# Kernel optimization log

Hardware: AMD Instinct MI355X
Metric: run time of the kernel (lower is better)

The kernel has to match this reference:

```python
import jax, jax.numpy as jnp
import numpy as np

DIM_X = 128
DIM_H = 128
HIDDEN = 512
BATCH = 4096


def _vf(x, h, t, W1, b1, W2, b2):
    # cfg vector field: 2-layer tanh MLP on concat([x, h, t]) -> (B, dim_x)
    B = x.shape[0]
    tcol = jnp.broadcast_to(jnp.reshape(t, (1, 1)), (B, 1)).astype(x.dtype)
    z = jnp.concatenate([x, h, tcol], axis=-1)  # (B, dim_x+dim_h+1)
    return jnp.tanh(z @ W1 + b1) @ W2 + b2  # (B, dim_x)


def _divergence(x, h, t, W1, b1, W2, b2):
    # Exact Jacobian trace: sum_i d v_i / d x_i, via dim_x forward-mode JVP
    # passes (replaces the torch per-dim reverse-mode autograd.grad loop).
    f = lambda xx: _vf(xx, h, t, W1, b1, W2, b2)
    dim = x.shape[1]

    def diag_i(i):
        e = jnp.zeros((dim,), x.dtype).at[i].set(1.0)
        _, tang = jax.jvp(f, (x,), (jnp.broadcast_to(e, x.shape),))  # (B, dim)
        return jnp.take(tang, i, axis=1)  # (B,)

    diag = jax.vmap(diag_i)(jnp.arange(dim))  # (dim, B)
    return jnp.sum(diag, axis=0)[:, None]  # (B, 1)


def setup_inputs() -> dict:
    key = jax.random.key(0)
    ks = jax.random.split(key, 9)
    return {
        "state": jax.random.normal(ks[0], (BATCH, DIM_X + 1), jnp.float32),
        "h": jax.random.normal(ks[1], (BATCH, DIM_H), jnp.float32),
        "h_null": jax.random.normal(ks[2], (BATCH, DIM_H), jnp.float32),
        "t": jax.random.uniform(ks[3], (1,), jnp.float32),
        "guidance_scale": jax.random.uniform(ks[4], (1,), jnp.float32),
        "W1": jax.random.normal(ks[5], (DIM_X + DIM_H + 1, HIDDEN), jnp.float32) * 0.05,
        "b1": jax.random.normal(ks[6], (HIDDEN,), jnp.float32) * 0.05,
        "W2": jax.random.normal(ks[7], (HIDDEN, DIM_X), jnp.float32) * 0.05,
        "b2": jax.random.normal(ks[8], (DIM_X,), jnp.float32) * 0.05,
    }


def reference(state, h, h_null, t, guidance_scale, W1, b1, W2, b2):
    x_t = state[:, :-1]  # (B, dim_x)
    gs = guidance_scale[0]
    v_h = _vf(x_t, h, t, W1, b1, W2, b2)
    v_h_null = _vf(x_t, h_null, t, W1, b1, W2, b2)
    v = (1.0 - gs) * v_h_null + gs * v_h
    div_h = _divergence(x_t, h, t, W1, b1, W2, b2)
    div_h_null = _divergence(x_t, h_null, t, W1, b1, W2, b2)
    div = (1.0 - gs) * div_h_null + gs * div_h
    return jnp.concatenate([v, div], axis=1)  # (B, dim_x+1)
```

## Files before the change

### kernel.cpp

```cpp
#include <hip/hip_runtime.h>
#include <hip/hip_bf16.h>

#define DX 128
#define DH 128
#define HID 512
#define NB 4096
#define ROWS 16
#define OUTC 129

typedef __attribute__((ext_vector_type(4))) float f32x4;
typedef __attribute__((ext_vector_type(4))) float float4v;
typedef __attribute__((ext_vector_type(2))) float float2v;
typedef __attribute__((ext_vector_type(8))) short bf16x8;
typedef __attribute__((ext_vector_type(4))) short bf16x4;
typedef __attribute__((ext_vector_type(2))) short bf16x2;

__device__ inline short f2bf(float f) {
    unsigned u = __float_as_uint(f);
    unsigned r = (u + 0x7fffu + ((u >> 16) & 1u)) >> 16;
    return (short)r;
}

__device__ inline float fast_tanh(float x) {
    float e = __expf(2.0f * x);
    float r = __builtin_amdgcn_rcpf(e + 1.0f);
    return 1.0f - 2.0f * r;
}

__global__ __launch_bounds__(256) void prep_kernel(
    const float* __restrict__ W1, const float* __restrict__ W2,
    float* __restrict__ c, short* __restrict__ w1p, short* __restrict__ w2p)
{
    __shared__ float tile[4][32][17];

    const int tid  = threadIdx.x;
    const int lane = tid & 63;
    const int w    = tid >> 6;
    const int l15  = lane & 15;
    const int l4   = lane >> 4;
    const int W    = blockIdx.x * 4 + w;

    if (W < 256) {
        int nt = W >> 3, ks = W & 7;
        int m0 = ks * 32, n0 = nt * 16;
        #pragma unroll
        for (int p = 0; p < 8; ++p) {
            int r = p * 4 + l4;
            tile[w][r][l15] = W1[(m0 + r) * HID + n0 + l15];
        }
    } else if (W < 384) {
        int idx = W - 256;
        int nt = idx >> 4, ks = idx & 15;
        int k0 = ks * 32, n0 = nt * 16;
        #pragma unroll
        for (int p = 0; p < 8; ++p) {
            int r = p * 4 + l4;
            tile[w][r][l15] = W2[(k0 + r) * DX + n0 + l15];
        }
    }
    __syncthreads();

    if (W < 256) {
        bf16x8 v;
        #pragma unroll
        for (int e = 0; e < 8; ++e) v[e] = f2bf(tile[w][l4 * 8 + e][l15]);
        *(bf16x8*)&w1p[W * 512 + lane * 8] = v;
    } else if (W < 384) {
        int idx = W - 256;
        bf16x8 v;
        #pragma unroll
        for (int e = 0; e < 8; ++e) v[e] = f2bf(tile[w][l4 * 8 + e][l15]);
        *(bf16x8*)&w2p[idx * 512 + lane * 8] = v;
    } else if (W < 896) {
        int k = W - 384;
        float p = W1[lane * HID + k] * W2[k * DX + lane]
                + W1[(lane + 64) * HID + k] * W2[k * DX + lane + 64];
        for (int m = 1; m < 64; m <<= 1) p += __shfl_xor(p, m, 64);
        if (lane == 0) c[k] = p;
    }
}

__global__ __launch_bounds__(1024) void cvf_kernel(
    const float* __restrict__ state, const float* __restrict__ h_,
    const float* __restrict__ hn_, const float* __restrict__ tptr,
    const float* __restrict__ gsptr, const float* __restrict__ W1,
    const float* __restrict__ b1, const float* __restrict__ b2,
    const float* __restrict__ c, const short* __restrict__ w1p,
    const short* __restrict__ w2p, float* __restrict__ out)
{
    __shared__ short xb [ROWS][DX  + 8];
    __shared__ short hb [ROWS][DH  + 8];
    __shared__ short hnb[ROWS][DH  + 8];
    __shared__ short ab_h[ROWS][HID + 8];
    __shared__ short ab_n[ROWS][HID + 8];
    __shared__ float divp[2][16][ROWS];

    const int tid  = threadIdx.x;
    const int lane = tid & 63;
    const int w    = tid >> 6;
    const int l15  = lane & 15;
    const int l4   = lane >> 4;
    const int row0 = blockIdx.x * ROWS;
    const float t  = tptr[0];
    const float gs = gsptr[0];

    bf16x8 bx[2][4];
    f32x4 base[2];
    #pragma unroll
    for (int j = 0; j < 2; ++j) {
        #pragma unroll
        for (int ks = 0; ks < 4; ++ks)
            bx[j][ks] = *(const bf16x8*)&w1p[(((w * 2 + j) * 8 + ks) * 64 + lane) * 8];
        int k0 = w * 32 + j * 16 + l4 * 4;
        float4v bb = *(const float4v*)&b1[k0];
        float4v tw = *(const float4v*)&W1[256 * HID + k0];
        #pragma unroll
        for (int q = 0; q < 4; ++q) base[j][q] = bb[q] + t * tw[q];
    }

    {
        int r  = tid >> 6;
        int c0 = (tid & 63) * 2;
        const float* sp = state + (row0 + r) * OUTC + c0;
        float2v vh = *(const float2v*)(h_  + (row0 + r) * DH + c0);
        float2v vn = *(const float2v*)(hn_ + (row0 + r) * DH + c0);
        bf16x2 sx, sh, sn;
        for (int e = 0; e < 2; ++e) {
            sx[e] = f2bf(sp[e]);
            sh[e] = f2bf(vh[e]);
            sn[e] = f2bf(vn[e]);
        }
        *(bf16x2*)&xb [r][c0] = sx;
        *(bf16x2*)&hb [r][c0] = sh;
        *(bf16x2*)&hnb[r][c0] = sn;
    }
    __syncthreads();

    f32x4 acc_h[2], acc_n[2];
    {
        bf16x8 ax[4];
        #pragma unroll
        for (int ks = 0; ks < 4; ++ks)
            ax[ks] = *(const bf16x8*)&xb[l15][ks * 32 + l4 * 8];

        f32x4 accx[2];
        #pragma unroll
        for (int j = 0; j < 2; ++j) accx[j] = base[j];
        #pragma unroll
        for (int ks = 0; ks < 4; ++ks)
            #pragma unroll
            for (int j = 0; j < 2; ++j)
                accx[j] = __builtin_amdgcn_mfma_f32_16x16x32_bf16(bx[j][ks], ax[ks], accx[j], 0, 0, 0);

        bf16x8 bh[2][4];
        #pragma unroll
        for (int j = 0; j < 2; ++j)
            #pragma unroll
            for (int ks = 0; ks < 4; ++ks)
                bh[j][ks] = *(const bf16x8*)&w1p[(((w * 2 + j) * 8 + 4 + ks) * 64 + lane) * 8];
        bf16x8 ah[4], an[4];
        #pragma unroll
        for (int ks = 0; ks < 4; ++ks) {
            ah[ks] = *(const bf16x8*)&hb [l15][ks * 32 + l4 * 8];
            an[ks] = *(const bf16x8*)&hnb[l15][ks * 32 + l4 * 8];
        }

        #pragma unroll
        for (int j = 0; j < 2; ++j) { acc_h[j] = accx[j]; acc_n[j] = accx[j]; }
        #pragma unroll
        for (int ks = 0; ks < 4; ++ks)
            #pragma unroll
            for (int j = 0; j < 2; ++j) {
                acc_h[j] = __builtin_amdgcn_mfma_f32_16x16x32_bf16(bh[j][ks], ah[ks], acc_h[j], 0, 0, 0);
                acc_n[j] = __builtin_amdgcn_mfma_f32_16x16x32_bf16(bh[j][ks], an[ks], acc_n[j], 0, 0, 0);
            }
    }

    bf16x8 b2f[8];
    if (w < 8) {
        #pragma unroll
        for (int ks = 0; ks < 8; ++ks)
            b2f[ks] = *(const bf16x8*)&w2p[((w * 16 + ks) * 64 + lane) * 8];
    }

    float dph = 0.f, dpn = 0.f;
    #pragma unroll
    for (int j = 0; j < 2; ++j) {
        int k0 = w * 32 + j * 16 + l4 * 4;
        float4v c4 = *(const float4v*)&c[k0];
        bf16x4 ph, pn;
        #pragma unroll
        for (int q = 0; q < 4; ++q) {
            float a1 = fast_tanh(acc_h[j][q]);
            float a2 = fast_tanh(acc_n[j][q]);
            ph[q] = f2bf(a1);
            pn[q] = f2bf(a2);
            dph += (1.f - a1 * a1) * c4[q];
            dpn += (1.f - a2 * a2) * c4[q];
        }
        *(bf16x4*)&ab_h[l15][k0] = ph;
        *(bf16x4*)&ab_n[l15][k0] = pn;
    }
    dph += __shfl_xor(dph, 16, 64);  dph += __shfl_xor(dph, 32, 64);
    dpn += __shfl_xor(dpn, 16, 64);  dpn += __shfl_xor(dpn, 32, 64);
    if (l4 == 0) {
        divp[0][w][l15] = dph;
        divp[1][w][l15] = dpn;
    }
    __syncthreads();

    if (w < 8) {
        f32x4 avh = (f32x4){0, 0, 0, 0}, avn = (f32x4){0, 0, 0, 0};
        #pragma unroll
        for (int ks = 0; ks < 8; ++ks) {
            bf16x8 afh = *(const bf16x8*)&ab_h[l15][ks * 32 + l4 * 8];
            bf16x8 afn = *(const bf16x8*)&ab_n[l15][ks * 32 + l4 * 8];
            avh = __builtin_amdgcn_mfma_f32_16x16x32_bf16(afh, b2f[ks], avh, 0, 0, 0);
            avn = __builtin_amdgcn_mfma_f32_16x16x32_bf16(afn, b2f[ks], avn, 0, 0, 0);
        }
        bf16x8 b2g[8];
        #pragma unroll
        for (int ks = 0; ks < 8; ++ks)
            b2g[ks] = *(const bf16x8*)&w2p[((w * 16 + 8 + ks) * 64 + lane) * 8];
        #pragma unroll
        for (int ks = 0; ks < 8; ++ks) {
            bf16x8 afh = *(const bf16x8*)&ab_h[l15][(8 + ks) * 32 + l4 * 8];
            bf16x8 afn = *(const bf16x8*)&ab_n[l15][(8 + ks) * 32 + l4 * 8];
            avh = __builtin_amdgcn_mfma_f32_16x16x32_bf16(afh, b2g[ks], avh, 0, 0, 0);
            avn = __builtin_amdgcn_mfma_f32_16x16x32_bf16(afn, b2g[ks], avn, 0, 0, 0);
        }
        int col = w * 16 + l15;
        float bb = b2[col];
        #pragma unroll
        for (int q = 0; q < 4; ++q) {
            int r = l4 * 4 + q;
            float v = (1.f - gs) * avn[q] + gs * avh[q] + bb;
            out[(row0 + r) * OUTC + col] = v;
        }
    } else if (w == 8 && lane < ROWS) {
        float dh = 0.f, dn = 0.f;
        #pragma unroll
        for (int ww = 0; ww < 16; ++ww) { dh += divp[0][ww][lane]; dn += divp[1][ww][lane]; }
        out[(row0 + lane) * OUTC + DX] = (1.f - gs) * dn + gs * dh;
    }
}

extern "C" void kernel_launch(void* const* d_in, const int* in_sizes, int n_in,
                              void* d_out, int out_size, void* d_ws, size_t ws_size,
                              hipStream_t stream) {
    const float* state = (const float*)d_in[0];
    const float* h     = (const float*)d_in[1];
    const float* hn    = (const float*)d_in[2];
    const float* t     = (const float*)d_in[3];
    const float* gs    = (const float*)d_in[4];
    const float* W1    = (const float*)d_in[5];
    const float* b1    = (const float*)d_in[6];
    const float* W2    = (const float*)d_in[7];
    const float* b2    = (const float*)d_in[8];
    float* out = (float*)d_out;

    float* c   = (float*)d_ws;
    short* w1p = (short*)((char*)d_ws + 2048);
    short* w2p = (short*)((char*)d_ws + 2048 + 262144);

    prep_kernel<<<224, 256, 0, stream>>>(W1, W2, c, w1p, w2p);
    cvf_kernel<<<NB / ROWS, 1024, 0, stream>>>(state, h, hn, t, gs, W1, b1, b2, c, w1p, w2p, out);
}
```

Before: 18.75 us.

## Fuse weight prep into main kernel and compute trace coefficients via MFMA

Drops the separate prep kernel that packed W1/W2 into bf16 MFMA layouts and computed the per-hidden-unit coefficient c[k] = sum_i W1[i,k]*W2[k,i]. Each block now loads fp32 W1/W2 straight from global memory with strided scalar reads and converts them in registers. It computes c through an extra MFMA of W1x against a transposed W2 tile staged in LDS, then extracts the diagonal with shuffles. This saves one kernel launch and a dependency, but every one of the 256 blocks repeats the weight conversion with uncoalesced strided loads, and c is now computed in bf16 precision.

```diff
diff --git a/kernel.cpp b/kernel.cpp
--- a/kernel.cpp
+++ b/kernel.cpp
@@ -10,7 +10,6 @@
 
 typedef __attribute__((ext_vector_type(4))) float f32x4;
 typedef __attribute__((ext_vector_type(4))) float float4v;
-typedef __attribute__((ext_vector_type(2))) float float2v;
 typedef __attribute__((ext_vector_type(8))) short bf16x8;
 typedef __attribute__((ext_vector_type(4))) short bf16x4;
 typedef __attribute__((ext_vector_type(2))) short bf16x2;
@@ -25,59 +24,6 @@
     float e = __expf(2.0f * x);
     float r = __builtin_amdgcn_rcpf(e + 1.0f);
     return 1.0f - 2.0f * r;
-}
-
-__global__ __launch_bounds__(256) void prep_kernel(
-    const float* __restrict__ W1, const float* __restrict__ W2,
-    float* __restrict__ c, short* __restrict__ w1p, short* __restrict__ w2p)
-{
-    __shared__ float tile[4][32][17];
-
-    const int tid  = threadIdx.x;
-    const int lane = tid & 63;
-    const int w    = tid >> 6;
-    const int l15  = lane & 15;
-    const int l4   = lane >> 4;
-    const int W    = blockIdx.x * 4 + w;
-
-    if (W < 256) {
-        int nt = W >> 3, ks = W & 7;
-        int m0 = ks * 32, n0 = nt * 16;
-        #pragma unroll
-        for (int p = 0; p < 8; ++p) {
-            int r = p * 4 + l4;
-            tile[w][r][l15] = W1[(m0 + r) * HID + n0 + l15];
-        }
-    } else if (W < 384) {
-        int idx = W - 256;
-        int nt = idx >> 4, ks = idx & 15;
-        int k0 = ks * 32, n0 = nt * 16;
-        #pragma unroll
-        for (int p = 0; p < 8; ++p) {
-            int r = p * 4 + l4;
-            tile[w][r][l15] = W2[(k0 + r) * DX + n0 + l15];
-        }
-    }
-    __syncthreads();
-
-    if (W < 256) {
-        bf16x8 v;
-        #pragma unroll
-        for (int e = 0; e < 8; ++e) v[e] = f2bf(tile[w][l4 * 8 + e][l15]);
-        *(bf16x8*)&w1p[W * 512 + lane * 8] = v;
-    } else if (W < 384) {
-        int idx = W - 256;
-        bf16x8 v;
-        #pragma unroll
-        for (int e = 0; e < 8; ++e) v[e] = f2bf(tile[w][l4 * 8 + e][l15]);
-        *(bf16x8*)&w2p[idx * 512 + lane * 8] = v;
-    } else if (W < 896) {
-        int k = W - 384;
-        float p = W1[lane * HID + k] * W2[k * DX + lane]
-                + W1[(lane + 64) * HID + k] * W2[k * DX + lane + 64];
-        for (int m = 1; m < 64; m <<= 1) p += __shfl_xor(p, m, 64);
-        if (lane == 0) c[k] = p;
-    }
 }
 
 __global__ __launch_bounds__(1024) void cvf_kernel(
@@ -85,12 +31,12 @@
     const float* __restrict__ hn_, const float* __restrict__ tptr,
     const float* __restrict__ gsptr, const float* __restrict__ W1,
     const float* __restrict__ b1, const float* __restrict__ b2,
-    const float* __restrict__ c, const short* __restrict__ w1p,
-    const short* __restrict__ w2p, float* __restrict__ out)
+    const float* __restrict__ W2, float* __restrict__ out)
 {
-    __shared__ short xb [ROWS][DX  + 8];
-    __shared__ short hb [ROWS][DH  + 8];
-    __shared__ short hnb[ROWS][DH  + 8];
+    __shared__ short tb [16][4][16][32];
+    __shared__ short xb [ROWS][DX + 8];
+    __shared__ short hb [ROWS][DH + 8];
+    __shared__ short hnb[ROWS][DH + 8];
     __shared__ short ab_h[ROWS][HID + 8];
     __shared__ short ab_n[ROWS][HID + 8];
     __shared__ float divp[2][16][ROWS];
@@ -104,13 +50,54 @@
     const float t  = tptr[0];
     const float gs = gsptr[0];
 
-    bf16x8 bx[2][4];
+    bf16x8 w2f[2][4];
+    #pragma unroll
+    for (int g = 0; g < 2; ++g) {
+        float4v tv[4][2];
+        #pragma unroll
+        for (int q2 = 0; q2 < 4; ++q2) {
+            int kt = 2 * w + g;
+            #pragma unroll
+            for (int p2 = 0; p2 < 2; ++p2) {
+                int r  = p2 * 8 + (lane >> 3);
+                int cc = (lane & 7) * 4;
+                tv[q2][p2] = *(const float4v*)&W2[(kt * 16 + r) * DX + q2 * 32 + cc];
+            }
+        }
+        #pragma unroll
+        for (int q2 = 0; q2 < 4; ++q2) {
+            #pragma unroll
+            for (int p2 = 0; p2 < 2; ++p2) {
+                int r  = p2 * 8 + (lane >> 3);
+                int cc = (lane & 7) * 4;
+                bf16x4 bv;
+                #pragma unroll
+                for (int e = 0; e < 4; ++e) bv[e] = f2bf(tv[q2][p2][e]);
+                *(bf16x4*)&tb[w][q2][r][cc] = bv;
+            }
+        }
+        #pragma unroll
+        for (int q2 = 0; q2 < 4; ++q2)
+            w2f[g][q2] = *(const bf16x8*)&tb[w][q2][l15][l4 * 8];
+    }
+
+    bf16x8 bx[2][4], bh[2][4];
     f32x4 base[2];
     #pragma unroll
     for (int j = 0; j < 2; ++j) {
-        #pragma unroll
-        for (int ks = 0; ks < 4; ++ks)
-            bx[j][ks] = *(const bf16x8*)&w1p[(((w * 2 + j) * 8 + ks) * 64 + lane) * 8];
+        int kcol = w * 32 + j * 16 + l15;
+        #pragma unroll
+        for (int ks = 0; ks < 4; ++ks) {
+            int mb = ks * 32 + l4 * 8;
+            bf16x8 vx, vh;
+            #pragma unroll
+            for (int e = 0; e < 8; ++e) {
+                vx[e] = f2bf(W1[(mb + e) * HID + kcol]);
+                vh[e] = f2bf(W1[(128 + mb + e) * HID + kcol]);
+            }
+            bx[j][ks] = vx;
+            bh[j][ks] = vh;
+        }
         int k0 = w * 32 + j * 16 + l4 * 4;
         float4v bb = *(const float4v*)&b1[k0];
         float4v tw = *(const float4v*)&W1[256 * HID + k0];
@@ -122,13 +109,14 @@
         int r  = tid >> 6;
         int c0 = (tid & 63) * 2;
         const float* sp = state + (row0 + r) * OUTC + c0;
-        float2v vh = *(const float2v*)(h_  + (row0 + r) * DH + c0);
-        float2v vn = *(const float2v*)(hn_ + (row0 + r) * DH + c0);
+        const float* hp = h_  + (row0 + r) * DH + c0;
+        const float* np = hn_ + (row0 + r) * DH + c0;
         bf16x2 sx, sh, sn;
+        #pragma unroll
         for (int e = 0; e < 2; ++e) {
             sx[e] = f2bf(sp[e]);
-            sh[e] = f2bf(vh[e]);
-            sn[e] = f2bf(vn[e]);
+            sh[e] = f2bf(hp[e]);
+            sn[e] = f2bf(np[e]);
         }
         *(bf16x2*)&xb [r][c0] = sx;
         *(bf16x2*)&hb [r][c0] = sh;
@@ -136,7 +124,7 @@
     }
     __syncthreads();
 
-    f32x4 acc_h[2], acc_n[2];
+    f32x4 acc_h[2], acc_n[2], Dc[2];
     {
         bf16x8 ax[4];
         #pragma unroll
@@ -145,26 +133,24 @@
 
         f32x4 accx[2];
         #pragma unroll
-        for (int j = 0; j < 2; ++j) accx[j] = base[j];
+        for (int j = 0; j < 2; ++j) {
+            accx[j] = base[j];
+            Dc[j]   = (f32x4){0, 0, 0, 0};
+        }
         #pragma unroll
         for (int ks = 0; ks < 4; ++ks)
             #pragma unroll
-            for (int j = 0; j < 2; ++j)
+            for (int j = 0; j < 2; ++j) {
                 accx[j] = __builtin_amdgcn_mfma_f32_16x16x32_bf16(bx[j][ks], ax[ks], accx[j], 0, 0, 0);
-
-        bf16x8 bh[2][4];
-        #pragma unroll
-        for (int j = 0; j < 2; ++j)
-            #pragma unroll
-            for (int ks = 0; ks < 4; ++ks)
-                bh[j][ks] = *(const bf16x8*)&w1p[(((w * 2 + j) * 8 + 4 + ks) * 64 + lane) * 8];
+                Dc[j]   = __builtin_amdgcn_mfma_f32_16x16x32_bf16(bx[j][ks], w2f[j][ks], Dc[j], 0, 0, 0);
+            }
+
         bf16x8 ah[4], an[4];
         #pragma unroll
         for (int ks = 0; ks < 4; ++ks) {
             ah[ks] = *(const bf16x8*)&hb [l15][ks * 32 + l4 * 8];
             an[ks] = *(const bf16x8*)&hnb[l15][ks * 32 + l4 * 8];
         }
-
         #pragma unroll
         for (int j = 0; j < 2; ++j) { acc_h[j] = accx[j]; acc_n[j] = accx[j]; }
         #pragma unroll
@@ -179,15 +165,23 @@
     bf16x8 b2f[8];
     if (w < 8) {
         #pragma unroll
-        for (int ks = 0; ks < 8; ++ks)
-            b2f[ks] = *(const bf16x8*)&w2p[((w * 16 + ks) * 64 + lane) * 8];
+        for (int ks = 0; ks < 8; ++ks) {
+            bf16x8 v;
+            #pragma unroll
+            for (int e = 0; e < 8; ++e)
+                v[e] = f2bf(W2[(ks * 32 + l4 * 8 + e) * DX + w * 16 + l15]);
+            b2f[ks] = v;
+        }
     }
 
     float dph = 0.f, dpn = 0.f;
     #pragma unroll
     for (int j = 0; j < 2; ++j) {
         int k0 = w * 32 + j * 16 + l4 * 4;
-        float4v c4 = *(const float4v*)&c[k0];
+        f32x4 c4;
+        #pragma unroll
+        for (int q = 0; q < 4; ++q)
+            c4[q] = __shfl(Dc[j][q], 20 * l4 + q, 64);
         bf16x4 ph, pn;
         #pragma unroll
         for (int q = 0; q < 4; ++q) {
@@ -220,8 +214,13 @@
         }
         bf16x8 b2g[8];
         #pragma unroll
-        for (int ks = 0; ks < 8; ++ks)
-            b2g[ks] = *(const bf16x8*)&w2p[((w * 16 + 8 + ks) * 64 + lane) * 8];
+        for (int ks = 0; ks < 8; ++ks) {
+            bf16x8 v;
+            #pragma unroll
+            for (int e = 0; e < 8; ++e)
+                v[e] = f2bf(W2[((8 + ks) * 32 + l4 * 8 + e) * DX + w * 16 + l15]);
+            b2g[ks] = v;
+        }
         #pragma unroll
         for (int ks = 0; ks < 8; ++ks) {
             bf16x8 afh = *(const bf16x8*)&ab_h[l15][(8 + ks) * 32 + l4 * 8];
@@ -259,10 +258,5 @@
     const float* b2    = (const float*)d_in[8];
     float* out = (float*)d_out;
 
-    float* c   = (float*)d_ws;
-    short* w1p = (short*)((char*)d_ws + 2048);
-    short* w2p = (short*)((char*)d_ws + 2048 + 262144);
-
-    prep_kernel<<<224, 256, 0, stream>>>(W1, W2, c, w1p, w2p);
-    cvf_kernel<<<NB / ROWS, 1024, 0, stream>>>(state, h, hn, t, gs, W1, b1, b2, c, w1p, w2p, out);
-}
+    cvf_kernel<<<NB / ROWS, 1024, 0, stream>>>(state, h, hn, t, gs, W1, b1, b2, W2, out);
+}
```

Result: slower. 43.60 us (+132.6%).

## Halve rows per block and widen per-wave hidden slice for more blocks

Applied to the files above, without the earlier changes.

Cuts the batch rows per block from 16 to 8 and launches 512-thread blocks, so twice as many blocks run. Each wave now covers 64 hidden units instead of 32, and all 8 waves join the second GEMM. The aim is better occupancy and less block-level serialization. The 16-row MFMA tiles are now half filled: the padding rows read neighbouring shared data and are discarded. That doubles the MFMA work and the weight loads per useful row.

```diff
diff --git a/kernel.cpp b/kernel.cpp
--- a/kernel.cpp
+++ b/kernel.cpp
@@ -5,7 +5,7 @@
 #define DH 128
 #define HID 512
 #define NB 4096
-#define ROWS 16
+#define ROWS 8
 #define OUTC 129
 
 typedef __attribute__((ext_vector_type(4))) float f32x4;
@@ -80,7 +80,7 @@
     }
 }
 
-__global__ __launch_bounds__(1024) void cvf_kernel(
+__global__ __launch_bounds__(512, 4) void cvf_kernel(
     const float* __restrict__ state, const float* __restrict__ h_,
     const float* __restrict__ hn_, const float* __restrict__ tptr,
     const float* __restrict__ gsptr, const float* __restrict__ W1,
@@ -88,12 +88,12 @@
     const float* __restrict__ c, const short* __restrict__ w1p,
     const short* __restrict__ w2p, float* __restrict__ out)
 {
-    __shared__ short xb [ROWS][DX  + 8];
-    __shared__ short hb [ROWS][DH  + 8];
-    __shared__ short hnb[ROWS][DH  + 8];
-    __shared__ short ab_h[ROWS][HID + 8];
-    __shared__ short ab_n[ROWS][HID + 8];
-    __shared__ float divp[2][16][ROWS];
+    __shared__ short xb [ROWS][DX + 8];
+    __shared__ short hb [ROWS][DH + 8];
+    __shared__ short hnb[ROWS][DH + 8];
+    __shared__ short ab_h[16][HID + 8];
+    __shared__ short ab_n[16][HID + 8];
+    __shared__ float divp[2][8][ROWS];
 
     const int tid  = threadIdx.x;
     const int lane = tid & 63;
@@ -104,14 +104,10 @@
     const float t  = tptr[0];
     const float gs = gsptr[0];
 
-    bf16x8 bx[2][4];
-    f32x4 base[2];
+    f32x4 base[4];
     #pragma unroll
-    for (int j = 0; j < 2; ++j) {
-        #pragma unroll
-        for (int ks = 0; ks < 4; ++ks)
-            bx[j][ks] = *(const bf16x8*)&w1p[(((w * 2 + j) * 8 + ks) * 64 + lane) * 8];
-        int k0 = w * 32 + j * 16 + l4 * 4;
+    for (int j = 0; j < 4; ++j) {
+        int k0 = w * 64 + j * 16 + l4 * 4;
         float4v bb = *(const float4v*)&b1[k0];
         float4v tw = *(const float4v*)&W1[256 * HID + k0];
         #pragma unroll
@@ -125,6 +121,7 @@
         float2v vh = *(const float2v*)(h_  + (row0 + r) * DH + c0);
         float2v vn = *(const float2v*)(hn_ + (row0 + r) * DH + c0);
         bf16x2 sx, sh, sn;
+        #pragma unroll
         for (int e = 0; e < 2; ++e) {
             sx[e] = f2bf(sp[e]);
             sh[e] = f2bf(vh[e]);
@@ -136,57 +133,44 @@
     }
     __syncthreads();
 
-    f32x4 acc_h[2], acc_n[2];
+    f32x4 acc_h[4], acc_n[4];
     {
-        bf16x8 ax[4];
-        #pragma unroll
-        for (int ks = 0; ks < 4; ++ks)
-            ax[ks] = *(const bf16x8*)&xb[l15][ks * 32 + l4 * 8];
-
-        f32x4 accx[2];
-        #pragma unroll
-        for (int j = 0; j < 2; ++j) accx[j] = base[j];
-        #pragma unroll
-        for (int ks = 0; ks < 4; ++ks)
+        f32x4 accx[4];
+        #pragma unroll
+        for (int j = 0; j < 4; ++j) accx[j] = base[j];
+        #pragma unroll
+        for (int ks = 0; ks < 4; ++ks) {
+            bf16x8 ax = *(const bf16x8*)&xb[l15][ks * 32 + l4 * 8];
             #pragma unroll
-            for (int j = 0; j < 2; ++j)
-                accx[j] = __builtin_amdgcn_mfma_f32_16x16x32_bf16(bx[j][ks], ax[ks], accx[j], 0, 0, 0);
-
-        bf16x8 bh[2][4];
-        #pragma unroll
-        for (int j = 0; j < 2; ++j)
+            for (int j = 0; j < 4; ++j) {
+                bf16x8 bxf = *(const bf16x8*)&w1p[(((w * 4 + j) * 8 + ks) * 64 + lane) * 8];
+                accx[j] = __builtin_amdgcn_mfma_f32_16x16x32_bf16(bxf, ax, accx[j], 0, 0, 0);
+            }
+        }
+        #pragma unroll
+        for (int j = 0; j < 4; ++j) { acc_h[j] = accx[j]; acc_n[j] = accx[j]; }
+        #pragma unroll
+        for (int ks = 0; ks < 4; ++ks) {
+            bf16x8 ah = *(const bf16x8*)&hb [l15][ks * 32 + l4 * 8];
+            bf16x8 an = *(const bf16x8*)&hnb[l15][ks * 32 + l4 * 8];
             #pragma unroll
-            for (int ks = 0; ks < 4; ++ks)
-                bh[j][ks] = *(const bf16x8*)&w1p[(((w * 2 + j) * 8 + 4 + ks) * 64 + lane) * 8];
-        bf16x8 ah[4], an[4];
-        #pragma unroll
-        for (int ks = 0; ks < 4; ++ks) {
-            ah[ks] = *(const bf16x8*)&hb [l15][ks * 32 + l4 * 8];
-            an[ks] = *(const bf16x8*)&hnb[l15][ks * 32 + l4 * 8];
-        }
-
-        #pragma unroll
-        for (int j = 0; j < 2; ++j) { acc_h[j] = accx[j]; acc_n[j] = accx[j]; }
-        #pragma unroll
-        for (int ks = 0; ks < 4; ++ks)
-            #pragma unroll
-            for (int j = 0; j < 2; ++j) {
-                acc_h[j] = __builtin_amdgcn_mfma_f32_16x16x32_bf16(bh[j][ks], ah[ks], acc_h[j], 0, 0, 0);
-                acc_n[j] = __builtin_amdgcn_mfma_f32_16x16x32_bf16(bh[j][ks], an[ks], acc_n[j], 0, 0, 0);
+            for (int j = 0; j < 4; ++j) {
+                bf16x8 bhf = *(const bf16x8*)&w1p[(((w * 4 + j) * 8 + 4 + ks) * 64 + lane) * 8];
+                acc_h[j] = __builtin_amdgcn_mfma_f32_16x16x32_bf16(bhf, ah, acc_h[j], 0, 0, 0);
+                acc_n[j] = __builtin_amdgcn_mfma_f32_16x16x32_bf16(bhf, an, acc_n[j], 0, 0, 0);
             }
+        }
     }
 
     bf16x8 b2f[8];
-    if (w < 8) {
-        #pragma unroll
-        for (int ks = 0; ks < 8; ++ks)
-            b2f[ks] = *(const bf16x8*)&w2p[((w * 16 + ks) * 64 + lane) * 8];
-    }
+    #pragma unroll
+    for (int ks = 0; ks < 8; ++ks)
+        b2f[ks] = *(const bf16x8*)&w2p[((w * 16 + ks) * 64 + lane) * 8];
 
     float dph = 0.f, dpn = 0.f;
     #pragma unroll
-    for (int j = 0; j < 2; ++j) {
-        int k0 = w * 32 + j * 16 + l4 * 4;
+    for (int j = 0; j < 4; ++j) {
+        int k0 = w * 64 + j * 16 + l4 * 4;
         float4v c4 = *(const float4v*)&c[k0];
         bf16x4 ph, pn;
         #pragma unroll
@@ -203,13 +187,13 @@
     }
     dph += __shfl_xor(dph, 16, 64);  dph += __shfl_xor(dph, 32, 64);
     dpn += __shfl_xor(dpn, 16, 64);  dpn += __shfl_xor(dpn, 32, 64);
-    if (l4 == 0) {
+    if (l4 == 0 && l15 < ROWS) {
         divp[0][w][l15] = dph;
         divp[1][w][l15] = dpn;
     }
     __syncthreads();
 
-    if (w < 8) {
+    {
         f32x4 avh = (f32x4){0, 0, 0, 0}, avn = (f32x4){0, 0, 0, 0};
         #pragma unroll
         for (int ks = 0; ks < 8; ++ks) {
@@ -229,18 +213,22 @@
             avh = __builtin_amdgcn_mfma_f32_16x16x32_bf16(afh, b2g[ks], avh, 0, 0, 0);
             avn = __builtin_amdgcn_mfma_f32_16x16x32_bf16(afn, b2g[ks], avn, 0, 0, 0);
         }
-        int col = w * 16 + l15;
-        float bb = b2[col];
-        #pragma unroll
-        for (int q = 0; q < 4; ++q) {
-            int r = l4 * 4 + q;
-            float v = (1.f - gs) * avn[q] + gs * avh[q] + bb;
-            out[(row0 + r) * OUTC + col] = v;
-        }
-    } else if (w == 8 && lane < ROWS) {
+        if (l4 < 2) {
+            int col = w * 16 + l15;
+            float bb = b2[col];
+            #pragma unroll
+            for (int q = 0; q < 4; ++q) {
+                int r = l4 * 4 + q;
+                float v = (1.f - gs) * avn[q] + gs * avh[q] + bb;
+                out[(row0 + r) * OUTC + col] = v;
+            }
+        }
+    }
+
+    if (w == 0 && lane < ROWS) {
         float dh = 0.f, dn = 0.f;
         #pragma unroll
-        for (int ww = 0; ww < 16; ++ww) { dh += divp[0][ww][lane]; dn += divp[1][ww][lane]; }
+        for (int ww = 0; ww < 8; ++ww) { dh += divp[0][ww][lane]; dn += divp[1][ww][lane]; }
         out[(row0 + lane) * OUTC + DX] = (1.f - gs) * dn + gs * dh;
     }
 }
@@ -264,5 +252,5 @@
     short* w2p = (short*)((char*)d_ws + 2048 + 262144);
 
     prep_kernel<<<224, 256, 0, stream>>>(W1, W2, c, w1p, w2p);
-    cvf_kernel<<<NB / ROWS, 1024, 0, stream>>>(state, h, hn, t, gs, W1, b1, b2, c, w1p, w2p, out);
-}
+    cvf_kernel<<<NB / ROWS, 512, 0, stream>>>(state, h, hn, t, gs, W1, b1, b2, c, w1p, w2p, out);
+}
```

New measurement: 22.18 us. 18.3% more time.

## Blend tanh activations before second GEMM and split K across all waves

Applied to the files above, without the earlier changes.

Because the second layer is linear, the guided and unguided hidden activations are blended with gs before the W2 product, which halves the second-layer MFMA work and the LDS activation buffer. The divergence terms are blended per element so only one partial sum is reduced. The second GEMM is also split along K across all 16 waves rather than 8, and the two K halves are combined through an extra LDS buffer and barrier. Rounding changes slightly because the blend now happens before the bf16 conversion instead of after the fp32 accumulation.

```diff
diff --git a/kernel.cpp b/kernel.cpp
--- a/kernel.cpp
+++ b/kernel.cpp
@@ -88,12 +88,12 @@
     const float* __restrict__ c, const short* __restrict__ w1p,
     const short* __restrict__ w2p, float* __restrict__ out)
 {
-    __shared__ short xb [ROWS][DX  + 8];
-    __shared__ short hb [ROWS][DH  + 8];
-    __shared__ short hnb[ROWS][DH  + 8];
-    __shared__ short ab_h[ROWS][HID + 8];
-    __shared__ short ab_n[ROWS][HID + 8];
-    __shared__ float divp[2][16][ROWS];
+    __shared__ short xb [ROWS][DX + 8];
+    __shared__ short hb [ROWS][DH + 8];
+    __shared__ short hnb[ROWS][DH + 8];
+    __shared__ short ab [ROWS][HID + 8];
+    __shared__ float divp[16][ROWS];
+    __shared__ float red[8][64][4];
 
     const int tid  = threadIdx.x;
     const int lane = tid & 63;
@@ -103,6 +103,7 @@
     const int row0 = blockIdx.x * ROWS;
     const float t  = tptr[0];
     const float gs = gsptr[0];
+    const float gn = 1.0f - gs;
 
     bf16x8 bx[2][4];
     f32x4 base[2];
@@ -125,6 +126,7 @@
         float2v vh = *(const float2v*)(h_  + (row0 + r) * DH + c0);
         float2v vn = *(const float2v*)(hn_ + (row0 + r) * DH + c0);
         bf16x2 sx, sh, sn;
+        #pragma unroll
         for (int e = 0; e < 2; ++e) {
             sx[e] = f2bf(sp[e]);
             sh[e] = f2bf(vh[e]);
@@ -176,72 +178,58 @@
             }
     }
 
+    const int nt2 = w >> 1;
+    const int ks0 = (w & 1) * 8;
     bf16x8 b2f[8];
-    if (w < 8) {
-        #pragma unroll
-        for (int ks = 0; ks < 8; ++ks)
-            b2f[ks] = *(const bf16x8*)&w2p[((w * 16 + ks) * 64 + lane) * 8];
-    }
-
-    float dph = 0.f, dpn = 0.f;
+    #pragma unroll
+    for (int ks = 0; ks < 8; ++ks)
+        b2f[ks] = *(const bf16x8*)&w2p[((nt2 * 16 + ks0 + ks) * 64 + lane) * 8];
+
+    float dp = 0.f;
     #pragma unroll
     for (int j = 0; j < 2; ++j) {
         int k0 = w * 32 + j * 16 + l4 * 4;
         float4v c4 = *(const float4v*)&c[k0];
-        bf16x4 ph, pn;
+        bf16x4 pb;
         #pragma unroll
         for (int q = 0; q < 4; ++q) {
             float a1 = fast_tanh(acc_h[j][q]);
             float a2 = fast_tanh(acc_n[j][q]);
-            ph[q] = f2bf(a1);
-            pn[q] = f2bf(a2);
-            dph += (1.f - a1 * a1) * c4[q];
-            dpn += (1.f - a2 * a2) * c4[q];
-        }
-        *(bf16x4*)&ab_h[l15][k0] = ph;
-        *(bf16x4*)&ab_n[l15][k0] = pn;
-    }
-    dph += __shfl_xor(dph, 16, 64);  dph += __shfl_xor(dph, 32, 64);
-    dpn += __shfl_xor(dpn, 16, 64);  dpn += __shfl_xor(dpn, 32, 64);
-    if (l4 == 0) {
-        divp[0][w][l15] = dph;
-        divp[1][w][l15] = dpn;
-    }
-    __syncthreads();
-
-    if (w < 8) {
-        f32x4 avh = (f32x4){0, 0, 0, 0}, avn = (f32x4){0, 0, 0, 0};
-        #pragma unroll
-        for (int ks = 0; ks < 8; ++ks) {
-            bf16x8 afh = *(const bf16x8*)&ab_h[l15][ks * 32 + l4 * 8];
-            bf16x8 afn = *(const bf16x8*)&ab_n[l15][ks * 32 + l4 * 8];
-            avh = __builtin_amdgcn_mfma_f32_16x16x32_bf16(afh, b2f[ks], avh, 0, 0, 0);
-            avn = __builtin_amdgcn_mfma_f32_16x16x32_bf16(afn, b2f[ks], avn, 0, 0, 0);
-        }
-        bf16x8 b2g[8];
-        #pragma unroll
-        for (int ks = 0; ks < 8; ++ks)
-            b2g[ks] = *(const bf16x8*)&w2p[((w * 16 + 8 + ks) * 64 + lane) * 8];
-        #pragma unroll
-        for (int ks = 0; ks < 8; ++ks) {
-            bf16x8 afh = *(const bf16x8*)&ab_h[l15][(8 + ks) * 32 + l4 * 8];
-            bf16x8 afn = *(const bf16x8*)&ab_n[l15][(8 + ks) * 32 + l4 * 8];
-            avh = __builtin_amdgcn_mfma_f32_16x16x32_bf16(afh, b2g[ks], avh, 0, 0, 0);
-            avn = __builtin_amdgcn_mfma_f32_16x16x32_bf16(afn, b2g[ks], avn, 0, 0, 0);
-        }
-        int col = w * 16 + l15;
+            pb[q] = f2bf(gs * a1 + gn * a2);
+            dp += (gs * (1.f - a1 * a1) + gn * (1.f - a2 * a2)) * c4[q];
+        }
+        *(bf16x4*)&ab[l15][k0] = pb;
+    }
+    dp += __shfl_xor(dp, 16, 64);
+    dp += __shfl_xor(dp, 32, 64);
+    if (l4 == 0) divp[w][l15] = dp;
+    __syncthreads();
+
+    f32x4 av = (f32x4){0, 0, 0, 0};
+    #pragma unroll
+    for (int ks = 0; ks < 8; ++ks) {
+        bf16x8 af = *(const bf16x8*)&ab[l15][(ks0 + ks) * 32 + l4 * 8];
+        av = __builtin_amdgcn_mfma_f32_16x16x32_bf16(af, b2f[ks], av, 0, 0, 0);
+    }
+    if (w & 1) {
+        #pragma unroll
+        for (int q = 0; q < 4; ++q) red[nt2][lane][q] = av[q];
+    }
+    __syncthreads();
+
+    if (!(w & 1)) {
+        int col = nt2 * 16 + l15;
         float bb = b2[col];
         #pragma unroll
         for (int q = 0; q < 4; ++q) {
             int r = l4 * 4 + q;
-            float v = (1.f - gs) * avn[q] + gs * avh[q] + bb;
-            out[(row0 + r) * OUTC + col] = v;
-        }
-    } else if (w == 8 && lane < ROWS) {
-        float dh = 0.f, dn = 0.f;
-        #pragma unroll
-        for (int ww = 0; ww < 16; ++ww) { dh += divp[0][ww][lane]; dn += divp[1][ww][lane]; }
-        out[(row0 + lane) * OUTC + DX] = (1.f - gs) * dn + gs * dh;
+            out[(row0 + r) * OUTC + col] = av[q] + red[nt2][lane][q] + bb;
+        }
+    } else if (w == 1 && lane < ROWS) {
+        float d = 0.f;
+        #pragma unroll
+        for (int ww = 0; ww < 16; ++ww) d += divp[ww][lane];
+        out[(row0 + lane) * OUTC + DX] = d;
     }
 }
 
```

Measured after the change: 17.57 us. 6.3% less time.
